# Optimization experiments

Measured on AMD Instinct MI355X. Metric: run time of the kernel, lower is better.

The kernel has to match this reference:

```python
import jax, jax.numpy as jnp
import numpy as np


def setup_inputs() -> dict:
    key = jax.random.key(0)
    ks = jax.random.split(key, 5)
    B, Lq, Lkv, HQ, H, D, S, BS = 1, 256, 4096, 32, 2, 128, 16, 64
    q = jax.random.normal(ks[0], (B, Lq, HQ, D), jnp.float32)
    k = jax.random.normal(ks[1], (B, Lkv, H, D), jnp.float32)
    v = jax.random.normal(ks[2], (B, Lkv, H, D), jnp.float32)
    w = jax.random.uniform(ks[3], (B, Lq, HQ, S), jnp.float32)
    block_indices = jax.random.randint(ks[4], (B, Lq, H, S), 0, Lkv // BS).astype(jnp.int32)
    return {"q": q, "k": k, "v": v, "w": w, "block_indices": block_indices, "block_size": BS}


def reference(q, k, v, w, block_indices, block_size):
    # q: (B, Lq, HQ, D); k,v: (B, Lkv, H, D); w: (B, Lq, HQ, num_weights);
    # block_indices: (B, Lq, H, S) int32, entries < 0 are skipped.
    B, Lq, HQ, D = q.shape
    H = k.shape[2]
    S = block_indices.shape[-1]
    G = HQ // H  # query heads per kv head
    nb = k.shape[1] // block_size
    sm_scale = 1.0 / (D ** 0.5)  # default scale in the kernel

    # Reshape KV into blocks: (B, H, nb, BS, D)
    kb = k.reshape(B, nb, block_size, H, D).transpose(0, 3, 1, 2, 4)
    vb = v.reshape(B, nb, block_size, H, D).transpose(0, 3, 1, 2, 4)

    idx = block_indices.transpose(0, 2, 1, 3)  # (B, H, Lq, S)
    valid = idx >= 0
    idx = jnp.maximum(idx, 0)

    # Gather selected blocks per (batch, kv_head): -> (B, H, Lq, S, BS, D)
    gather = jax.vmap(jax.vmap(lambda blocks, ind: blocks[ind]))
    kg = gather(kb, idx)
    vg = gather(vb, idx)

    # Group query heads by kv head: (B, H, Lq, G, D)
    qh = q.reshape(B, Lq, H, G, D).transpose(0, 2, 1, 3, 4)

    # Per-block scores and per-block softmax over the BS keys (axis u)
    scores = jnp.einsum('bhlgd,bhlsud->bhlgsu', qh, kg) * sm_scale
    p = jax.nn.softmax(scores, axis=-1)

    # Per-(head, block) learned weight; only first S weights of w are used.
    wh = w[..., :S].reshape(B, Lq, H, G, S).transpose(0, 2, 1, 3, 4)  # (B,H,Lq,G,S)
    coef = wh * valid[:, :, :, None, :].astype(p.dtype)
    p = p * coef[..., None]

    o = jnp.einsum('bhlgsu,bhlsud->bhlgd', p, vg)  # (B, H, Lq, G, D)
    return o.transpose(0, 2, 1, 3, 4).reshape(B, Lq, HQ, D)
```

## Files before the change

kernel.cpp:

```cpp
#include <hip/hip_runtime.h>
#include <hip/hip_bf16.h>


namespace {

constexpr int kLq = 256, kHQ = 32, kH = 2, kG = 16, kD = 128, kS = 16;
constexpr int kNB = 64;
constexpr float kScaleLog2e = 0.08838834764831845f * 1.4426950408889634f;

constexpr int kKPackN = kH * kNB * 16 * 64;
constexpr int kPStr   = 72;
constexpr int kSStr   = 136;

constexpr int kQOff = 0;
constexpr int kPOff = 32768;

typedef short s16x8 __attribute__((ext_vector_type(8)));
typedef float f32x4 __attribute__((ext_vector_type(4)));

union U32BF2 { unsigned int u; __hip_bfloat162 h; };
union FragU  { uint4 u; s16x8 v; };

static __device__ inline unsigned int pk_bf16(float a, float b) {
    U32BF2 z; z.h = __float22bfloat162_rn(make_float2(a, b));
    return z.u;
}

__global__ __launch_bounds__(256)
void pack_kv(const float* __restrict__ k, const float* __restrict__ v,
             uint4* __restrict__ kp, uint4* __restrict__ vp)
{
    __shared__ unsigned short S_s[32 * kSStr];

    const int bid  = blockIdx.x;
    const int isV  = bid & 1;
    const int half = (bid >> 1) & 1;
    const int blk  = (bid >> 2) & 63;
    const int h    = bid >> 8;
    const int t    = threadIdx.x;
    const int lane = t & 63, n = lane & 15, quad = lane >> 4;
    const int wv   = t >> 6;

    {
        const float* src = (isV ? v : k) +
            ((size_t)(blk * 64 + half * 32) * kH + h) * kD;
        const int r0 = t >> 5, c4 = (t & 31) << 2;
        #pragma unroll
        for (int p = 0; p < 4; ++p) {
            const int r = p * 8 + r0;
            const f32x4 f = __builtin_nontemporal_load(
                (const f32x4*)(src + (size_t)r * (kH * kD) + c4));
            *(unsigned int*)&S_s[r * kSStr + c4]     = pk_bf16(f[0], f[1]);
            *(unsigned int*)&S_s[r * kSStr + c4 + 2] = pk_bf16(f[2], f[3]);
        }
    }
    __syncthreads();

    const size_t obase = (size_t)(h * 64 + blk) * 16 * 64;
    if (!isV) {
        #pragma unroll
        for (int rep = 0; rep < 2; ++rep) {
            const int cl    = wv * 2 + rep;
            const int t_loc = cl >> 2, st = cl & 3;
            const int c     = (2 * half + t_loc) * 4 + st;
            const int u_loc = t_loc * 16 + n;
            kp[obase + (size_t)c * 64 + lane] =
                *(const uint4*)&S_s[u_loc * kSStr + st * 32 + quad * 8];
        }
    } else {
        #pragma unroll
        for (int rep = 0; rep < 2; ++rep) {
            const int dt = wv * 2 + rep;
            const int c  = dt * 2 + half;
            const int d  = dt * 16 + n;
            unsigned short s[8];
            #pragma unroll
            for (int j = 0; j < 8; ++j) s[j] = S_s[(quad * 8 + j) * kSStr + d];
            uint4 val;
            val.x = s[0] | ((unsigned)s[1] << 16);
            val.y = s[2] | ((unsigned)s[3] << 16);
            val.z = s[4] | ((unsigned)s[5] << 16);
            val.w = s[6] | ((unsigned)s[7] << 16);
            vp[obase + (size_t)c * 64 + lane] = val;
        }
    }
}

__global__ __launch_bounds__(512, 4)
void hsa_main(const float* __restrict__ q, const float* __restrict__ w,
              const int* __restrict__ bidx, const uint4* __restrict__ kp,
              const uint4* __restrict__ vp, float* __restrict__ out)
{
    __shared__ __align__(16) unsigned char smem[69632];

    const int bid  = blockIdx.x;
    const int xcd  = bid & 7;
    const int h    = xcd >> 2;
    const int l    = (bid >> 3) * 4 + (xcd & 3);
    const int tid  = threadIdx.x;
    const int wave = tid >> 6;
    const int lane = tid & 63;
    const int n    = lane & 15;
    const int quad = lane >> 4;

    unsigned char* qlds = smem + kQOff + wave * 4096 + lane * 16;
    {
        const float* qb = q + ((size_t)l * kHQ + h * kG + n) * kD + quad * 8;
        #pragma unroll
        for (int st = 0; st < 4; ++st) {
            const f32x4 f0 = __builtin_nontemporal_load((const f32x4*)(qb + st * 32));
            const f32x4 f1 = __builtin_nontemporal_load((const f32x4*)(qb + st * 32 + 4));
            uint4 z;
            z.x = pk_bf16(f0[0], f0[1]); z.y = pk_bf16(f0[2], f0[3]);
            z.z = pk_bf16(f1[0], f1[1]); z.w = pk_bf16(f1[2], f1[3]);
            *(uint4*)(qlds + st * 1024) = z;
        }
    }

    int   baseA, baseB;
    float wvalA, wvalB;
    {
        const int sA = wave * 2, sB = wave * 2 + 1;
        const int biA = bidx[(size_t)(l * kH + h) * kS + sA];
        const int biB = bidx[(size_t)(l * kH + h) * kS + sB];
        wvalA = (biA < 0) ? 0.f : w[((size_t)l * kHQ + h * kG + n) * kS + sA];
        wvalB = (biB < 0) ? 0.f : w[((size_t)l * kHQ + h * kG + n) * kS + sB];
        baseA = (h * kNB + max(biA, 0)) * 1024;
        baseB = (h * kNB + max(biB, 0)) * 1024;
    }

    unsigned short* PA = (unsigned short*)(smem + kPOff + wave * 4608);
    unsigned short* PB = PA + kG * kPStr;

    FragU kA[4], kB[4], vrA[4], vrB[4];
    #pragma unroll
    for (int st = 0; st < 4; ++st) kA[st].u = kp[baseA + st * 64 + lane];
    #pragma unroll
    for (int st = 0; st < 4; ++st) kB[st].u = kp[baseB + st * 64 + lane];
    #pragma unroll
    for (int i = 0; i < 4; ++i)    vrA[i].u = vp[baseA + i * 64 + lane];
    #pragma unroll
    for (int i = 0; i < 4; ++i)    vrB[i].u = vp[baseA + (4 + i) * 64 + lane];
    __builtin_amdgcn_sched_barrier(0);

    f32x4 oacc[8];
    #pragma unroll
    for (int dt = 0; dt < 8; ++dt) oacc[dt] = (f32x4){0.f, 0.f, 0.f, 0.f};

    float partA = 0.f, partB = 0.f;
    #pragma unroll
    for (int t = 0; t < 4; ++t) {
        {
            f32x4 sc = {0.f, 0.f, 0.f, 0.f};
            #pragma unroll
            for (int st = 0; st < 4; ++st) {
                const s16x8 aq = *(const s16x8*)(qlds + st * 1024);
                sc = __builtin_amdgcn_mfma_f32_16x16x32_bf16(kA[st].v, aq, sc, 0, 0, 0);
            }
            if (t < 3) {
                #pragma unroll
                for (int st = 0; st < 4; ++st)
                    kA[st].u = kp[baseA + ((t + 1) * 4 + st) * 64 + lane];
            }
            __builtin_amdgcn_sched_barrier(0);
            #pragma unroll
            for (int r = 0; r < 4; ++r) {
                sc[r] = exp2f(sc[r] * kScaleLog2e);
                partA += sc[r];
            }
            const unsigned long long pq =
                ((unsigned long long)pk_bf16(sc[2], sc[3]) << 32) | pk_bf16(sc[0], sc[1]);
            *(unsigned long long*)&PA[n * kPStr + t * 16 + quad * 4] = pq;
        }
        {
            f32x4 sc = {0.f, 0.f, 0.f, 0.f};
            #pragma unroll
            for (int st = 0; st < 4; ++st) {
                const s16x8 aq = *(const s16x8*)(qlds + st * 1024);
                sc = __builtin_amdgcn_mfma_f32_16x16x32_bf16(kB[st].v, aq, sc, 0, 0, 0);
            }
            if (t < 3) {
                #pragma unroll
                for (int st = 0; st < 4; ++st)
                    kB[st].u = kp[baseB + ((t + 1) * 4 + st) * 64 + lane];
            }
            __builtin_amdgcn_sched_barrier(0);
            #pragma unroll
            for (int r = 0; r < 4; ++r) {
                sc[r] = exp2f(sc[r] * kScaleLog2e);
                partB += sc[r];
            }
            const unsigned long long pq =
                ((unsigned long long)pk_bf16(sc[2], sc[3]) << 32) | pk_bf16(sc[0], sc[1]);
            *(unsigned long long*)&PB[n * kPStr + t * 16 + quad * 4] = pq;
        }
    }

    partA += __shfl_xor(partA, 16);
    partA += __shfl_xor(partA, 32);
    partB += __shfl_xor(partB, 16);
    partB += __shfl_xor(partB, 32);
    const float coefA = wvalA / partA;
    const float coefB = wvalB / partB;

    const f32x4 zero = {0.f, 0.f, 0.f, 0.f};

    {
        const s16x8 bf0 = *(const s16x8*)&PA[n * kPStr + quad * 8];
        const s16x8 bf1 = *(const s16x8*)&PA[n * kPStr + 32 + quad * 8];

        {
            f32x4 p0 = __builtin_amdgcn_mfma_f32_16x16x32_bf16(vrA[0].v, bf0, zero, 0, 0, 0);
            p0       = __builtin_amdgcn_mfma_f32_16x16x32_bf16(vrA[1].v, bf1, p0,   0, 0, 0);
            f32x4 p1 = __builtin_amdgcn_mfma_f32_16x16x32_bf16(vrA[2].v, bf0, zero, 0, 0, 0);
            p1       = __builtin_amdgcn_mfma_f32_16x16x32_bf16(vrA[3].v, bf1, p1,   0, 0, 0);
            #pragma unroll
            for (int i = 0; i < 4; ++i) vrA[i].u = vp[baseA + (8 + i) * 64 + lane];
            __builtin_amdgcn_sched_barrier(0);
            #pragma unroll
            for (int r = 0; r < 4; ++r) {
                oacc[0][r] = fmaf(coefA, p0[r], oacc[0][r]);
                oacc[1][r] = fmaf(coefA, p1[r], oacc[1][r]);
            }
        }
        {
            f32x4 p0 = __builtin_amdgcn_mfma_f32_16x16x32_bf16(vrB[0].v, bf0, zero, 0, 0, 0);
            p0       = __builtin_amdgcn_mfma_f32_16x16x32_bf16(vrB[1].v, bf1, p0,   0, 0, 0);
            f32x4 p1 = __builtin_amdgcn_mfma_f32_16x16x32_bf16(vrB[2].v, bf0, zero, 0, 0, 0);
            p1       = __builtin_amdgcn_mfma_f32_16x16x32_bf16(vrB[3].v, bf1, p1,   0, 0, 0);
            #pragma unroll
            for (int i = 0; i < 4; ++i) vrB[i].u = vp[baseA + (12 + i) * 64 + lane];
            __builtin_amdgcn_sched_barrier(0);
            #pragma unroll
            for (int r = 0; r < 4; ++r) {
                oacc[2][r] = fmaf(coefA, p0[r], oacc[2][r]);
                oacc[3][r] = fmaf(coefA, p1[r], oacc[3][r]);
            }
        }
        {
            f32x4 p0 = __builtin_amdgcn_mfma_f32_16x16x32_bf16(vrA[0].v, bf0, zero, 0, 0, 0);
            p0       = __builtin_amdgcn_mfma_f32_16x16x32_bf16(vrA[1].v, bf1, p0,   0, 0, 0);
            f32x4 p1 = __builtin_amdgcn_mfma_f32_16x16x32_bf16(vrA[2].v, bf0, zero, 0, 0, 0);
            p1       = __builtin_amdgcn_mfma_f32_16x16x32_bf16(vrA[3].v, bf1, p1,   0, 0, 0);
            #pragma unroll
            for (int i = 0; i < 4; ++i) vrA[i].u = vp[baseB + i * 64 + lane];
            __builtin_amdgcn_sched_barrier(0);
            #pragma unroll
            for (int r = 0; r < 4; ++r) {
                oacc[4][r] = fmaf(coefA, p0[r], oacc[4][r]);
                oacc[5][r] = fmaf(coefA, p1[r], oacc[5][r]);
            }
        }
        {
            f32x4 p0 = __builtin_amdgcn_mfma_f32_16x16x32_bf16(vrB[0].v, bf0, zero, 0, 0, 0);
            p0       = __builtin_amdgcn_mfma_f32_16x16x32_bf16(vrB[1].v, bf1, p0,   0, 0, 0);
            f32x4 p1 = __builtin_amdgcn_mfma_f32_16x16x32_bf16(vrB[2].v, bf0, zero, 0, 0, 0);
            p1       = __builtin_amdgcn_mfma_f32_16x16x32_bf16(vrB[3].v, bf1, p1,   0, 0, 0);
            #pragma unroll
            for (int i = 0; i < 4; ++i) vrB[i].u = vp[baseB + (4 + i) * 64 + lane];
            __builtin_amdgcn_sched_barrier(0);
            #pragma unroll
            for (int r = 0; r < 4; ++r) {
                oacc[6][r] = fmaf(coefA, p0[r], oacc[6][r]);
                oacc[7][r] = fmaf(coefA, p1[r], oacc[7][r]);
            }
        }
    }

    {
        const s16x8 bf0 = *(const s16x8*)&PB[n * kPStr + quad * 8];
        const s16x8 bf1 = *(const s16x8*)&PB[n * kPStr + 32 + quad * 8];

        {
            f32x4 p0 = __builtin_amdgcn_mfma_f32_16x16x32_bf16(vrA[0].v, bf0, zero, 0, 0, 0);
            p0       = __builtin_amdgcn_mfma_f32_16x16x32_bf16(vrA[1].v, bf1, p0,   0, 0, 0);
            f32x4 p1 = __builtin_amdgcn_mfma_f32_16x16x32_bf16(vrA[2].v, bf0, zero, 0, 0, 0);
            p1       = __builtin_amdgcn_mfma_f32_16x16x32_bf16(vrA[3].v, bf1, p1,   0, 0, 0);
            #pragma unroll
            for (int i = 0; i < 4; ++i) vrA[i].u = vp[baseB + (8 + i) * 64 + lane];
            __builtin_amdgcn_sched_barrier(0);
            #pragma unroll
            for (int r = 0; r < 4; ++r) {
                oacc[0][r] = fmaf(coefB, p0[r], oacc[0][r]);
                oacc[1][r] = fmaf(coefB, p1[r], oacc[1][r]);
            }
        }
        {
            f32x4 p0 = __builtin_amdgcn_mfma_f32_16x16x32_bf16(vrB[0].v, bf0, zero, 0, 0, 0);
            p0       = __builtin_amdgcn_mfma_f32_16x16x32_bf16(vrB[1].v, bf1, p0,   0, 0, 0);
            f32x4 p1 = __builtin_amdgcn_mfma_f32_16x16x32_bf16(vrB[2].v, bf0, zero, 0, 0, 0);
            p1       = __builtin_amdgcn_mfma_f32_16x16x32_bf16(vrB[3].v, bf1, p1,   0, 0, 0);
            #pragma unroll
            for (int i = 0; i < 4; ++i) vrB[i].u = vp[baseB + (12 + i) * 64 + lane];
            __builtin_amdgcn_sched_barrier(0);
            #pragma unroll
            for (int r = 0; r < 4; ++r) {
                oacc[2][r] = fmaf(coefB, p0[r], oacc[2][r]);
                oacc[3][r] = fmaf(coefB, p1[r], oacc[3][r]);
            }
        }
        {
            f32x4 p0 = __builtin_amdgcn_mfma_f32_16x16x32_bf16(vrA[0].v, bf0, zero, 0, 0, 0);
            p0       = __builtin_amdgcn_mfma_f32_16x16x32_bf16(vrA[1].v, bf1, p0,   0, 0, 0);
            f32x4 p1 = __builtin_amdgcn_mfma_f32_16x16x32_bf16(vrA[2].v, bf0, zero, 0, 0, 0);
            p1       = __builtin_amdgcn_mfma_f32_16x16x32_bf16(vrA[3].v, bf1, p1,   0, 0, 0);
            #pragma unroll
            for (int r = 0; r < 4; ++r) {
                oacc[4][r] = fmaf(coefB, p0[r], oacc[4][r]);
                oacc[5][r] = fmaf(coefB, p1[r], oacc[5][r]);
            }
        }
        {
            f32x4 p0 = __builtin_amdgcn_mfma_f32_16x16x32_bf16(vrB[0].v, bf0, zero, 0, 0, 0);
            p0       = __builtin_amdgcn_mfma_f32_16x16x32_bf16(vrB[1].v, bf1, p0,   0, 0, 0);
            f32x4 p1 = __builtin_amdgcn_mfma_f32_16x16x32_bf16(vrB[2].v, bf0, zero, 0, 0, 0);
            p1       = __builtin_amdgcn_mfma_f32_16x16x32_bf16(vrB[3].v, bf1, p1,   0, 0, 0);
            #pragma unroll
            for (int r = 0; r < 4; ++r) {
                oacc[6][r] = fmaf(coefB, p0[r], oacc[6][r]);
                oacc[7][r] = fmaf(coefB, p1[r], oacc[7][r]);
            }
        }
    }

    __syncthreads();
    float* epi = (float*)(smem + kQOff);

    if (wave >= 4) {
        #pragma unroll
        for (int dt = 0; dt < 8; ++dt)
            *(f32x4*)&epi[(wave - 4) * 2048 + dt * 256 + lane * 4] = oacc[dt];
    }
    __syncthreads();
    if (wave < 4) {
        #pragma unroll
        for (int dt = 0; dt < 8; ++dt) {
            const f32x4 o = *(const f32x4*)&epi[wave * 2048 + dt * 256 + lane * 4];
            #pragma unroll
            for (int r = 0; r < 4; ++r) oacc[dt][r] += o[r];
        }
    }
    __syncthreads();
    if (wave == 2 || wave == 3) {
        #pragma unroll
        for (int dt = 0; dt < 8; ++dt)
            *(f32x4*)&epi[(wave - 2) * 2048 + dt * 256 + lane * 4] = oacc[dt];
    }
    __syncthreads();
    if (wave < 2) {
        #pragma unroll
        for (int dt = 0; dt < 8; ++dt) {
            const f32x4 o = *(const f32x4*)&epi[wave * 2048 + dt * 256 + lane * 4];
            #pragma unroll
            for (int r = 0; r < 4; ++r) oacc[dt][r] += o[r];
        }
    }
    __syncthreads();
    if (wave == 1) {
        #pragma unroll
        for (int dt = 0; dt < 8; ++dt)
            *(f32x4*)&epi[dt * 256 + lane * 4] = oacc[dt];
    }
    __syncthreads();
    if (wave == 0) {
        float* ob = out + ((size_t)l * kHQ + h * kG + n) * kD;
        #pragma unroll
        for (int dt = 0; dt < 8; ++dt) {
            const f32x4 o = *(const f32x4*)&epi[dt * 256 + lane * 4];
            f32x4 val;
            #pragma unroll
            for (int r = 0; r < 4; ++r) val[r] = oacc[dt][r] + o[r];
            __builtin_nontemporal_store(val, (f32x4*)(ob + dt * 16 + quad * 4));
        }
    }
}

}

extern "C" void kernel_launch(void* const* d_in, const int* in_sizes, int n_in,
                              void* d_out, int out_size, void* d_ws, size_t ws_size,
                              hipStream_t stream)
{
    const float* q    = (const float*)d_in[0];
    const float* k    = (const float*)d_in[1];
    const float* v    = (const float*)d_in[2];
    const float* w    = (const float*)d_in[3];
    const int*   bidx = (const int*)d_in[4];
    float* out = (float*)d_out;

    uint4* kp = (uint4*)d_ws;
    uint4* vp = (uint4*)((char*)d_ws + (size_t)kKPackN * 16);

    pack_kv<<<dim3(512), dim3(256), 0, stream>>>(k, v, kp, vp);
    hsa_main<<<dim3(kLq * kH), dim3(512), 0, stream>>>(q, w, bidx, kp, vp, out);
}
```

Baseline: 89.59 us.

## Fuse KV packing and attention into one kernel with a grid barrier

Merges the separate KV pack kernel into the main attention kernel. Each of the 512 blocks packs a slice of K/V to bf16 and then waits at a global atomic epoch barrier before running attention. This removes one kernel launch and the inter-kernel gap. The cost is a software grid-wide barrier whose correctness depends on all 512 blocks being co-resident; the launch bounds of 4 blocks per CU make that plausible on this GPU.

```diff
diff --git a/kernel.cpp b/kernel.cpp
--- a/kernel.cpp
+++ b/kernel.cpp
@@ -11,6 +11,7 @@
 constexpr int kKPackN = kH * kNB * 16 * 64;
 constexpr int kPStr   = 72;
 constexpr int kSStr   = 136;
+constexpr int kGrid   = 512;
 
 constexpr int kQOff = 0;
 constexpr int kPOff = 32768;
@@ -26,51 +27,56 @@
     return z.u;
 }
 
-__global__ __launch_bounds__(256)
-void pack_kv(const float* __restrict__ k, const float* __restrict__ v,
-             uint4* __restrict__ kp, uint4* __restrict__ vp)
+__device__ int g_arrive = 0;
+__device__ int g_epoch  = 0;
+
+__global__ __launch_bounds__(512, 4)
+void hsa_fused(const float* __restrict__ q, const float* __restrict__ k,
+               const float* __restrict__ v, const float* __restrict__ w,
+               const int* __restrict__ bidx, uint4* __restrict__ kp,
+               uint4* __restrict__ vp, float* __restrict__ out)
 {
-    __shared__ unsigned short S_s[32 * kSStr];
+    __shared__ __align__(16) unsigned char smem[69632];
 
     const int bid  = blockIdx.x;
-    const int isV  = bid & 1;
-    const int half = (bid >> 1) & 1;
-    const int blk  = (bid >> 2) & 63;
-    const int h    = bid >> 8;
-    const int t    = threadIdx.x;
-    const int lane = t & 63, n = lane & 15, quad = lane >> 4;
-    const int wv   = t >> 6;
+    const int tid  = threadIdx.x;
+    const int wave = tid >> 6;
+    const int lane = tid & 63;
+    const int n    = lane & 15;
+    const int quad = lane >> 4;
 
     {
-        const float* src = (isV ? v : k) +
-            ((size_t)(blk * 64 + half * 32) * kH + h) * kD;
-        const int r0 = t >> 5, c4 = (t & 31) << 2;
-        #pragma unroll
-        for (int p = 0; p < 4; ++p) {
-            const int r = p * 8 + r0;
-            const f32x4 f = __builtin_nontemporal_load(
-                (const f32x4*)(src + (size_t)r * (kH * kD) + c4));
-            *(unsigned int*)&S_s[r * kSStr + c4]     = pk_bf16(f[0], f[1]);
-            *(unsigned int*)&S_s[r * kSStr + c4 + 2] = pk_bf16(f[2], f[3]);
-        }
-    }
-    __syncthreads();
-
-    const size_t obase = (size_t)(h * 64 + blk) * 16 * 64;
-    if (!isV) {
-        #pragma unroll
-        for (int rep = 0; rep < 2; ++rep) {
-            const int cl    = wv * 2 + rep;
-            const int t_loc = cl >> 2, st = cl & 3;
+        unsigned short* S_s = (unsigned short*)smem;
+        const int isV  = bid & 1;
+        const int half = (bid >> 1) & 1;
+        const int blk  = (bid >> 2) & 63;
+        const int hh   = bid >> 8;
+        const int wv8  = tid >> 6;
+
+        {
+            const float* src = (isV ? v : k) +
+                ((size_t)(blk * 64 + half * 32) * kH + hh) * kD;
+            const int r0 = tid >> 5, c4 = (tid & 31) << 2;
+            #pragma unroll
+            for (int p = 0; p < 2; ++p) {
+                const int r = p * 16 + r0;
+                const f32x4 f = __builtin_nontemporal_load(
+                    (const f32x4*)(src + (size_t)r * (kH * kD) + c4));
+                *(unsigned int*)&S_s[r * kSStr + c4]     = pk_bf16(f[0], f[1]);
+                *(unsigned int*)&S_s[r * kSStr + c4 + 2] = pk_bf16(f[2], f[3]);
+            }
+        }
+        __syncthreads();
+
+        const size_t obase = (size_t)(hh * 64 + blk) * 16 * 64;
+        if (!isV) {
+            const int t_loc = wv8 >> 2, st = wv8 & 3;
             const int c     = (2 * half + t_loc) * 4 + st;
             const int u_loc = t_loc * 16 + n;
             kp[obase + (size_t)c * 64 + lane] =
                 *(const uint4*)&S_s[u_loc * kSStr + st * 32 + quad * 8];
-        }
-    } else {
-        #pragma unroll
-        for (int rep = 0; rep < 2; ++rep) {
-            const int dt = wv * 2 + rep;
+        } else {
+            const int dt = wv8;
             const int c  = dt * 2 + half;
             const int d  = dt * 16 + n;
             unsigned short s[8];
@@ -84,24 +90,26 @@
             vp[obase + (size_t)c * 64 + lane] = val;
         }
     }
-}
-
-__global__ __launch_bounds__(512, 4)
-void hsa_main(const float* __restrict__ q, const float* __restrict__ w,
-              const int* __restrict__ bidx, const uint4* __restrict__ kp,
-              const uint4* __restrict__ vp, float* __restrict__ out)
-{
-    __shared__ __align__(16) unsigned char smem[69632];
-
-    const int bid  = blockIdx.x;
-    const int xcd  = bid & 7;
-    const int h    = xcd >> 2;
-    const int l    = (bid >> 3) * 4 + (xcd & 3);
-    const int tid  = threadIdx.x;
-    const int wave = tid >> 6;
-    const int lane = tid & 63;
-    const int n    = lane & 15;
-    const int quad = lane >> 4;
+
+    __syncthreads();
+    if (tid == 0) {
+        __threadfence();
+        const int a  = __hip_atomic_fetch_add(&g_arrive, 1, __ATOMIC_ACQ_REL,
+                                              __HIP_MEMORY_SCOPE_AGENT);
+        const int ep = a / kGrid;
+        if ((a % kGrid) == kGrid - 1)
+            __hip_atomic_fetch_add(&g_epoch, 1, __ATOMIC_ACQ_REL,
+                                   __HIP_MEMORY_SCOPE_AGENT);
+        while (__hip_atomic_load(&g_epoch, __ATOMIC_ACQUIRE,
+                                 __HIP_MEMORY_SCOPE_AGENT) <= ep)
+            __builtin_amdgcn_s_sleep(2);
+        __threadfence();
+    }
+    __syncthreads();
+
+    const int xcd = bid & 7;
+    const int h   = xcd >> 2;
+    const int l   = (bid >> 3) * 4 + (xcd & 3);
 
     unsigned char* qlds = smem + kQOff + wave * 4096 + lane * 16;
     {
@@ -391,6 +399,5 @@
     uint4* kp = (uint4*)d_ws;
     uint4* vp = (uint4*)((char*)d_ws + (size_t)kKPackN * 16);
 
-    pack_kv<<<dim3(512), dim3(256), 0, stream>>>(k, v, kp, vp);
-    hsa_main<<<dim3(kLq * kH), dim3(512), 0, stream>>>(q, w, bidx, kp, vp, out);
+    hsa_fused<<<dim3(kGrid), dim3(512), 0, stream>>>(q, k, v, w, bidx, kp, vp, out);
 }
```

Measured after the change: 144.7 us. 1.62x slower.

## Split PV stage by output D-tile per wave instead of by KV block

Applied to the files above, without the earlier changes.

Waves still compute scores for their own two KV blocks, but the PV product is repartitioned so each wave owns one 16-wide slice of D and loops over all 16 blocks, reading P tiles and per-block coefficients from shared memory. This removes the multi-stage cross-wave LDS reduction of full output accumulators, cuts per-wave V register footprint, and shrinks shared memory (Q stored once rather than per wave). It adds a block-wide barrier before PV and more LDS reads of P, and pads the P stride to reduce bank conflicts.

```diff
diff --git a/kernel.cpp b/kernel.cpp
--- a/kernel.cpp
+++ b/kernel.cpp
@@ -9,11 +9,14 @@
 constexpr float kScaleLog2e = 0.08838834764831845f * 1.4426950408889634f;
 
 constexpr int kKPackN = kH * kNB * 16 * 64;
-constexpr int kPStr   = 72;
+constexpr int kPStr   = 74;
+constexpr int kPBlk   = 16 * kPStr;
+constexpr int kPWave  = 2 * kPBlk;
 constexpr int kSStr   = 136;
 
-constexpr int kQOff = 0;
-constexpr int kPOff = 32768;
+constexpr int kCoefOff = 0;
+constexpr int kQOff    = 1024;
+constexpr int kPOff    = 5120;
 
 typedef short s16x8 __attribute__((ext_vector_type(8)));
 typedef float f32x4 __attribute__((ext_vector_type(4)));
@@ -91,7 +94,7 @@
               const int* __restrict__ bidx, const uint4* __restrict__ kp,
               const uint4* __restrict__ vp, float* __restrict__ out)
 {
-    __shared__ __align__(16) unsigned char smem[69632];
+    __shared__ __align__(16) unsigned char smem[43008];
 
     const int bid  = blockIdx.x;
     const int xcd  = bid & 7;
@@ -103,7 +106,10 @@
     const int n    = lane & 15;
     const int quad = lane >> 4;
 
-    unsigned char* qlds = smem + kQOff + wave * 4096 + lane * 16;
+    const int bv     = bidx[(size_t)(l * kH + h) * kS + n];
+    const int baseSv = (h * kNB + max(bv, 0)) * 1024;
+
+    unsigned char* qlds = smem + kQOff + lane * 16;
     {
         const float* qb = q + ((size_t)l * kHQ + h * kG + n) * kD + quad * 8;
         #pragma unroll
@@ -117,35 +123,25 @@
         }
     }
 
-    int   baseA, baseB;
-    float wvalA, wvalB;
-    {
-        const int sA = wave * 2, sB = wave * 2 + 1;
-        const int biA = bidx[(size_t)(l * kH + h) * kS + sA];
-        const int biB = bidx[(size_t)(l * kH + h) * kS + sB];
-        wvalA = (biA < 0) ? 0.f : w[((size_t)l * kHQ + h * kG + n) * kS + sA];
-        wvalB = (biB < 0) ? 0.f : w[((size_t)l * kHQ + h * kG + n) * kS + sB];
-        baseA = (h * kNB + max(biA, 0)) * 1024;
-        baseB = (h * kNB + max(biB, 0)) * 1024;
-    }
-
-    unsigned short* PA = (unsigned short*)(smem + kPOff + wave * 4608);
-    unsigned short* PB = PA + kG * kPStr;
-
-    FragU kA[4], kB[4], vrA[4], vrB[4];
+    const int sA = wave * 2, sB = wave * 2 + 1;
+    const int biA = __builtin_amdgcn_readlane(bv, sA);
+    const int biB = __builtin_amdgcn_readlane(bv, sB);
+    const int baseA = __builtin_amdgcn_readlane(baseSv, sA);
+    const int baseB = __builtin_amdgcn_readlane(baseSv, sB);
+    const float wvalA =
+        (biA < 0) ? 0.f : w[((size_t)l * kHQ + h * kG + n) * kS + sA];
+    const float wvalB =
+        (biB < 0) ? 0.f : w[((size_t)l * kHQ + h * kG + n) * kS + sB];
+
+    unsigned short* PA = (unsigned short*)(smem + kPOff) + wave * kPWave;
+    unsigned short* PB = PA + kPBlk;
+
+    FragU kA[4], kB[4];
     #pragma unroll
     for (int st = 0; st < 4; ++st) kA[st].u = kp[baseA + st * 64 + lane];
     #pragma unroll
     for (int st = 0; st < 4; ++st) kB[st].u = kp[baseB + st * 64 + lane];
-    #pragma unroll
-    for (int i = 0; i < 4; ++i)    vrA[i].u = vp[baseA + i * 64 + lane];
-    #pragma unroll
-    for (int i = 0; i < 4; ++i)    vrB[i].u = vp[baseA + (4 + i) * 64 + lane];
     __builtin_amdgcn_sched_barrier(0);
-
-    f32x4 oacc[8];
-    #pragma unroll
-    for (int dt = 0; dt < 8; ++dt) oacc[dt] = (f32x4){0.f, 0.f, 0.f, 0.f};
 
     float partA = 0.f, partB = 0.f;
     #pragma unroll
@@ -196,183 +192,53 @@
         }
     }
 
+    const int cOff0 = wave * 2 * 64 + lane;
+    const int cOff1 = cOff0 + 64;
+    FragU v0[4], v1[4];
+    #pragma unroll
+    for (int s = 0; s < 4; ++s) {
+        const int bs = __builtin_amdgcn_readlane(baseSv, s);
+        v0[s].u = vp[bs + cOff0];
+        v1[s].u = vp[bs + cOff1];
+    }
+    __builtin_amdgcn_sched_barrier(0);
+
     partA += __shfl_xor(partA, 16);
     partA += __shfl_xor(partA, 32);
     partB += __shfl_xor(partB, 16);
     partB += __shfl_xor(partB, 32);
-    const float coefA = wvalA / partA;
-    const float coefB = wvalB / partB;
+    float* coefT = (float*)(smem + kCoefOff);
+    if (quad == 0) {
+        coefT[sA * 16 + n] = wvalA / partA;
+        coefT[sB * 16 + n] = wvalB / partB;
+    }
+
+    __syncthreads();
 
     const f32x4 zero = {0.f, 0.f, 0.f, 0.f};
-
-    {
-        const s16x8 bf0 = *(const s16x8*)&PA[n * kPStr + quad * 8];
-        const s16x8 bf1 = *(const s16x8*)&PA[n * kPStr + 32 + quad * 8];
-
-        {
-            f32x4 p0 = __builtin_amdgcn_mfma_f32_16x16x32_bf16(vrA[0].v, bf0, zero, 0, 0, 0);
-            p0       = __builtin_amdgcn_mfma_f32_16x16x32_bf16(vrA[1].v, bf1, p0,   0, 0, 0);
-            f32x4 p1 = __builtin_amdgcn_mfma_f32_16x16x32_bf16(vrA[2].v, bf0, zero, 0, 0, 0);
-            p1       = __builtin_amdgcn_mfma_f32_16x16x32_bf16(vrA[3].v, bf1, p1,   0, 0, 0);
-            #pragma unroll
-            for (int i = 0; i < 4; ++i) vrA[i].u = vp[baseA + (8 + i) * 64 + lane];
-            __builtin_amdgcn_sched_barrier(0);
-            #pragma unroll
-            for (int r = 0; r < 4; ++r) {
-                oacc[0][r] = fmaf(coefA, p0[r], oacc[0][r]);
-                oacc[1][r] = fmaf(coefA, p1[r], oacc[1][r]);
-            }
-        }
-        {
-            f32x4 p0 = __builtin_amdgcn_mfma_f32_16x16x32_bf16(vrB[0].v, bf0, zero, 0, 0, 0);
-            p0       = __builtin_amdgcn_mfma_f32_16x16x32_bf16(vrB[1].v, bf1, p0,   0, 0, 0);
-            f32x4 p1 = __builtin_amdgcn_mfma_f32_16x16x32_bf16(vrB[2].v, bf0, zero, 0, 0, 0);
-            p1       = __builtin_amdgcn_mfma_f32_16x16x32_bf16(vrB[3].v, bf1, p1,   0, 0, 0);
-            #pragma unroll
-            for (int i = 0; i < 4; ++i) vrB[i].u = vp[baseA + (12 + i) * 64 + lane];
-            __builtin_amdgcn_sched_barrier(0);
-            #pragma unroll
-            for (int r = 0; r < 4; ++r) {
-                oacc[2][r] = fmaf(coefA, p0[r], oacc[2][r]);
-                oacc[3][r] = fmaf(coefA, p1[r], oacc[3][r]);
-            }
-        }
-        {
-            f32x4 p0 = __builtin_amdgcn_mfma_f32_16x16x32_bf16(vrA[0].v, bf0, zero, 0, 0, 0);
-            p0       = __builtin_amdgcn_mfma_f32_16x16x32_bf16(vrA[1].v, bf1, p0,   0, 0, 0);
-            f32x4 p1 = __builtin_amdgcn_mfma_f32_16x16x32_bf16(vrA[2].v, bf0, zero, 0, 0, 0);
-            p1       = __builtin_amdgcn_mfma_f32_16x16x32_bf16(vrA[3].v, bf1, p1,   0, 0, 0);
-            #pragma unroll
-            for (int i = 0; i < 4; ++i) vrA[i].u = vp[baseB + i * 64 + lane];
-            __builtin_amdgcn_sched_barrier(0);
-            #pragma unroll
-            for (int r = 0; r < 4; ++r) {
-                oacc[4][r] = fmaf(coefA, p0[r], oacc[4][r]);
-                oacc[5][r] = fmaf(coefA, p1[r], oacc[5][r]);
-            }
-        }
-        {
-            f32x4 p0 = __builtin_amdgcn_mfma_f32_16x16x32_bf16(vrB[0].v, bf0, zero, 0, 0, 0);
-            p0       = __builtin_amdgcn_mfma_f32_16x16x32_bf16(vrB[1].v, bf1, p0,   0, 0, 0);
-            f32x4 p1 = __builtin_amdgcn_mfma_f32_16x16x32_bf16(vrB[2].v, bf0, zero, 0, 0, 0);
-            p1       = __builtin_amdgcn_mfma_f32_16x16x32_bf16(vrB[3].v, bf1, p1,   0, 0, 0);
-            #pragma unroll
-            for (int i = 0; i < 4; ++i) vrB[i].u = vp[baseB + (4 + i) * 64 + lane];
-            __builtin_amdgcn_sched_barrier(0);
-            #pragma unroll
-            for (int r = 0; r < 4; ++r) {
-                oacc[6][r] = fmaf(coefA, p0[r], oacc[6][r]);
-                oacc[7][r] = fmaf(coefA, p1[r], oacc[7][r]);
-            }
-        }
-    }
-
-    {
-        const s16x8 bf0 = *(const s16x8*)&PB[n * kPStr + quad * 8];
-        const s16x8 bf1 = *(const s16x8*)&PB[n * kPStr + 32 + quad * 8];
-
-        {
-            f32x4 p0 = __builtin_amdgcn_mfma_f32_16x16x32_bf16(vrA[0].v, bf0, zero, 0, 0, 0);
-            p0       = __builtin_amdgcn_mfma_f32_16x16x32_bf16(vrA[1].v, bf1, p0,   0, 0, 0);
-            f32x4 p1 = __builtin_amdgcn_mfma_f32_16x16x32_bf16(vrA[2].v, bf0, zero, 0, 0, 0);
-            p1       = __builtin_amdgcn_mfma_f32_16x16x32_bf16(vrA[3].v, bf1, p1,   0, 0, 0);
-            #pragma unroll
-            for (int i = 0; i < 4; ++i) vrA[i].u = vp[baseB + (8 + i) * 64 + lane];
-            __builtin_amdgcn_sched_barrier(0);
-            #pragma unroll
-            for (int r = 0; r < 4; ++r) {
-                oacc[0][r] = fmaf(coefB, p0[r], oacc[0][r]);
-                oacc[1][r] = fmaf(coefB, p1[r], oacc[1][r]);
-            }
-        }
-        {
-            f32x4 p0 = __builtin_amdgcn_mfma_f32_16x16x32_bf16(vrB[0].v, bf0, zero, 0, 0, 0);
-            p0       = __builtin_amdgcn_mfma_f32_16x16x32_bf16(vrB[1].v, bf1, p0,   0, 0, 0);
-            f32x4 p1 = __builtin_amdgcn_mfma_f32_16x16x32_bf16(vrB[2].v, bf0, zero, 0, 0, 0);
-            p1       = __builtin_amdgcn_mfma_f32_16x16x32_bf16(vrB[3].v, bf1, p1,   0, 0, 0);
-            #pragma unroll
-            for (int i = 0; i < 4; ++i) vrB[i].u = vp[baseB + (12 + i) * 64 + lane];
-            __builtin_amdgcn_sched_barrier(0);
-            #pragma unroll
-            for (int r = 0; r < 4; ++r) {
-                oacc[2][r] = fmaf(coefB, p0[r], oacc[2][r]);
-                oacc[3][r] = fmaf(coefB, p1[r], oacc[3][r]);
-            }
-        }
-        {
-            f32x4 p0 = __builtin_amdgcn_mfma_f32_16x16x32_bf16(vrA[0].v, bf0, zero, 0, 0, 0);
-            p0       = __builtin_amdgcn_mfma_f32_16x16x32_bf16(vrA[1].v, bf1, p0,   0, 0, 0);
-            f32x4 p1 = __builtin_amdgcn_mfma_f32_16x16x32_bf16(vrA[2].v, bf0, zero, 0, 0, 0);
-            p1       = __builtin_amdgcn_mfma_f32_16x16x32_bf16(vrA[3].v, bf1, p1,   0, 0, 0);
-            #pragma unroll
-            for (int r = 0; r < 4; ++r) {
-                oacc[4][r] = fmaf(coefB, p0[r], oacc[4][r]);
-                oacc[5][r] = fmaf(coefB, p1[r], oacc[5][r]);
-            }
-        }
-        {
-            f32x4 p0 = __builtin_amdgcn_mfma_f32_16x16x32_bf16(vrB[0].v, bf0, zero, 0, 0, 0);
-            p0       = __builtin_amdgcn_mfma_f32_16x16x32_bf16(vrB[1].v, bf1, p0,   0, 0, 0);
-            f32x4 p1 = __builtin_amdgcn_mfma_f32_16x16x32_bf16(vrB[2].v, bf0, zero, 0, 0, 0);
-            p1       = __builtin_amdgcn_mfma_f32_16x16x32_bf16(vrB[3].v, bf1, p1,   0, 0, 0);
-            #pragma unroll
-            for (int r = 0; r < 4; ++r) {
-                oacc[6][r] = fmaf(coefB, p0[r], oacc[6][r]);
-                oacc[7][r] = fmaf(coefB, p1[r], oacc[7][r]);
-            }
-        }
-    }
-
-    __syncthreads();
-    float* epi = (float*)(smem + kQOff);
-
-    if (wave >= 4) {
-        #pragma unroll
-        for (int dt = 0; dt < 8; ++dt)
-            *(f32x4*)&epi[(wave - 4) * 2048 + dt * 256 + lane * 4] = oacc[dt];
-    }
-    __syncthreads();
-    if (wave < 4) {
-        #pragma unroll
-        for (int dt = 0; dt < 8; ++dt) {
-            const f32x4 o = *(const f32x4*)&epi[wave * 2048 + dt * 256 + lane * 4];
-            #pragma unroll
-            for (int r = 0; r < 4; ++r) oacc[dt][r] += o[r];
-        }
-    }
-    __syncthreads();
-    if (wave == 2 || wave == 3) {
-        #pragma unroll
-        for (int dt = 0; dt < 8; ++dt)
-            *(f32x4*)&epi[(wave - 2) * 2048 + dt * 256 + lane * 4] = oacc[dt];
-    }
-    __syncthreads();
-    if (wave < 2) {
-        #pragma unroll
-        for (int dt = 0; dt < 8; ++dt) {
-            const f32x4 o = *(const f32x4*)&epi[wave * 2048 + dt * 256 + lane * 4];
-            #pragma unroll
-            for (int r = 0; r < 4; ++r) oacc[dt][r] += o[r];
-        }
-    }
-    __syncthreads();
-    if (wave == 1) {
-        #pragma unroll
-        for (int dt = 0; dt < 8; ++dt)
-            *(f32x4*)&epi[dt * 256 + lane * 4] = oacc[dt];
-    }
-    __syncthreads();
-    if (wave == 0) {
-        float* ob = out + ((size_t)l * kHQ + h * kG + n) * kD;
-        #pragma unroll
-        for (int dt = 0; dt < 8; ++dt) {
-            const f32x4 o = *(const f32x4*)&epi[dt * 256 + lane * 4];
-            f32x4 val;
-            #pragma unroll
-            for (int r = 0; r < 4; ++r) val[r] = oacc[dt][r] + o[r];
-            __builtin_nontemporal_store(val, (f32x4*)(ob + dt * 16 + quad * 4));
-        }
-    }
+    f32x4 oacc = zero;
+    #pragma unroll
+    for (int s = 0; s < 16; ++s) {
+        const int slot = s & 3;
+        const unsigned short* Ps =
+            (const unsigned short*)(smem + kPOff) + (s >> 1) * kPWave + (s & 1) * kPBlk;
+        const s16x8 bf0 = *(const s16x8*)&Ps[n * kPStr + quad * 8];
+        const s16x8 bf1 = *(const s16x8*)&Ps[n * kPStr + 32 + quad * 8];
+        const float c   = coefT[s * 16 + n];
+        f32x4 p = __builtin_amdgcn_mfma_f32_16x16x32_bf16(v0[slot].v, bf0, zero, 0, 0, 0);
+        p       = __builtin_amdgcn_mfma_f32_16x16x32_bf16(v1[slot].v, bf1, p,    0, 0, 0);
+        if (s < 12) {
+            const int bs = __builtin_amdgcn_readlane(baseSv, s + 4);
+            v0[slot].u = vp[bs + cOff0];
+            v1[slot].u = vp[bs + cOff1];
+        }
+        __builtin_amdgcn_sched_barrier(0);
+        #pragma unroll
+        for (int r = 0; r < 4; ++r) oacc[r] = fmaf(c, p[r], oacc[r]);
+    }
+
+    float* ob = out + ((size_t)l * kHQ + h * kG + n) * kD + wave * 16 + quad * 4;
+    __builtin_nontemporal_store(oacc, (f32x4*)ob);
 }
 
 }
```

After: 99.27 us. +10.8%, slower.
